# Performance work log

Hardware: AMD Instinct MI355X
Metric: run time of the kernel (lower is better)

The kernel has to match this reference:

```python
import jax, jax.numpy as jnp
import numpy as np

THRESHOLD = 0.9
N = 20000
K = 32
F = 64


def setup_inputs() -> dict:
    key = jax.random.key(0)
    k1, k2, k3, k4, k5 = jax.random.split(key, 5)
    features = jax.random.normal(k1, (N, F), dtype=jnp.float32)
    score = jax.random.normal(k2, (N, 1), dtype=jnp.float32)
    distances = jax.random.uniform(k3, (N, K), dtype=jnp.float32)
    # two equal segments; neighbours sampled within own segment, self at col 0
    row_splits = jnp.array([0, N // 2, N], dtype=jnp.int32)
    segN = N // 2
    local_self = (jnp.arange(N, dtype=jnp.int32) % segN)
    seg_start = (jnp.arange(N, dtype=jnp.int32) // segN) * segN
    r = jax.random.randint(k4, (N, K - 1), 0, segN - 1, dtype=jnp.int32)
    r = r + (r >= local_self[:, None]).astype(jnp.int32)  # avoid sampling self
    neigh = seg_start[:, None] + r
    nidxs = jnp.concatenate([jnp.arange(N, dtype=jnp.int32)[:, None], neigh], axis=1)
    tidxs = jax.random.randint(k5, (N, 1), 0, 50, dtype=jnp.int32)
    return {"features": features, "score": score, "distances": distances,
            "nidxs": nidxs, "row_splits": row_splits, "tidxs": tidxs}


def _lnc(features, score_logits, nidxs, row_splits):
    n, k = nidxs.shape
    score = jax.nn.sigmoid(score_logits[:, 0])  # [N]
    # hierarchy order: per row-split segment, descending score
    seg_id = jnp.searchsorted(row_splits, jnp.arange(n), side='right') - 1
    order = jnp.lexsort((-score, seg_id))

    arangeK = jnp.arange(k)

    def step(carry, p):
        ggather, sel, npg, gcount = carry
        already = ggather[p] >= 0
        high = score[p] > THRESHOLD
        m = nidxs[p]                                   # [K], m[0] == p (self)
        free = (m >= 0) & (ggather[jnp.clip(m, 0, n - 1)] < 0)
        self_only = arangeK == 0
        valid = jnp.where(high, free, self_only) & (~already) & (m >= 0)
        g = gcount
        idx_w = jnp.where(valid, m, n)                 # dummy slot n for masked writes
        ggather = ggather.at[idx_w].set(g)
        row_i = jnp.where(already, n, g)
        sel = sel.at[row_i].set(jnp.where(valid, m, -1))
        npg = npg.at[row_i].set(jnp.sum(valid.astype(jnp.int32)))
        created = (~already).astype(jnp.int32)
        return (ggather, sel, npg, gcount + created), created

    init = (jnp.full((n + 1,), -1, jnp.int32),
            jnp.full((n + 1, k), -1, jnp.int32),
            jnp.zeros((n + 1,), jnp.int32),
            jnp.int32(0))
    (ggather, sel, npg, gcount), created = jax.lax.scan(step, init, order)
    ggather, sel, npg = ggather[:n], sel[:n], npg[:n]

    # new row splits: cumulative group count at segment boundaries
    cum = jnp.cumsum(created)
    rs_new = jnp.concatenate([jnp.zeros((1,), jnp.int32),
                              cum[row_splits[1:] - 1].astype(jnp.int32)])

    # pooled features per group (rows >= gcount are padding)
    sel_c = jnp.clip(sel, 0, n - 1)
    gathered = features[sel_c]                         # [N, K, F]
    mask = (sel >= 0)[..., None]
    out_mean = jnp.sum(jnp.where(mask, gathered, 0.0), axis=1)
    out_mean = out_mean / (npg[:, None].astype(features.dtype) + 1e-6)
    out_max = jnp.max(jnp.where(mask, gathered, -1000.0), axis=1)
    out = jnp.concatenate([out_mean, out_max], axis=-1)  # [N, 2F]
    backgather = ggather[:, None]
    return out, rs_new, backgather


def reference(features, score, distances, nidxs, row_splits, tidxs):
    # distances/tidxs only feed the (disabled) loss branch; kept for signature parity
    return _lnc(features, score, nidxs, row_splits)
```

## Files before the change

kernel.cpp:

```cpp
#include <hip/hip_runtime.h>


constexpr int KN = 32;
constexpr int FD = 64;
constexpr int HOCAP = 512;
constexpr int EW = 16;
constexpr int NBB = 2048;
constexpr int NT = 256;
constexpr int NMAX = 20000;
constexpr int BSLOT = 64;

typedef unsigned long long u64;


__global__ void k0_init(const float* __restrict__ score, float* __restrict__ s,
                        int* __restrict__ grab, u64* __restrict__ hlkStage,
                        int* __restrict__ hcnt, int* __restrict__ lcnt0,
                        int* __restrict__ lcnt1, u64* __restrict__ key,
                        const int* __restrict__ row_splits, int n) {
  __shared__ int ch, cl0, cl1;
  int tid = (int)threadIdx.x, bid = (int)blockIdx.x;
  int x = bid * NT + tid;
  int lane = tid & 63;
  int half = row_splits[1];
  if (tid == 0) { ch = 0; cl0 = 0; cl1 = 0; }
  __syncthreads();
  bool hi = false, lo = false;
  u64 pk = 0;
  if (x < n) {
    float sp = 1.0f / (1.0f + expf(-score[x]));
    s[x] = sp; grab[x] = 0x7FFFFFFF;
    hi = sp > 0.9f; lo = !hi;
    unsigned sb = __float_as_uint(sp);
    pk = ((u64)(x >= half) << 63) | ((u64)(0x7FFFFFFFu - sb) << 32) | (unsigned)x;
    key[x] = lo ? (((u64)sb << 32) | (u64)(0xFFFFFFFFu - (unsigned)x)) : 0ull;
  }
  u64 bh = __ballot(hi);
  u64 b0 = __ballot(lo && x < half);
  u64 b1 = __ballot(lo && x >= half);
  int base = 0;
  if (lane == 0) {
    if (bh) base = atomicAdd(&ch, __popcll(bh));
    if (b0) atomicAdd(&cl0, __popcll(b0));
    if (b1) atomicAdd(&cl1, __popcll(b1));
  }
  base = __shfl(base, 0);
  if (hi) {
    int idx = base + __popcll(bh & ((1ull << lane) - 1ull));
    if (idx < BSLOT) hlkStage[bid * BSLOT + idx] = pk;
  }
  __syncthreads();
  if (tid == 0) {
    hcnt[bid] = (ch > BSLOT) ? BSLOT : ch;
    lcnt0[bid] = cl0; lcnt1[bid] = cl1;
  }
}

__global__ __launch_bounds__(1024, 1) void kA(
    const u64* __restrict__ hlkStage, const int* __restrict__ hcnt,
    const int* __restrict__ lcnt0, const int* __restrict__ lcnt1,
    const int* __restrict__ nidxs, const int* __restrict__ row_splits,
    int* __restrict__ nbm, int* __restrict__ fgj, int* __restrict__ counters,
    int n) {
  __shared__ unsigned short hr16[NMAX];
  __shared__ unsigned E[HOCAP * EW];
  __shared__ u64 hk[HOCAP];
  __shared__ int hol[HOCAP];
  __shared__ int fgjL[HOCAP];
  __shared__ int cnts[128];
  __shared__ int pref[129];
  __shared__ int lsum[2];
  __shared__ int shg;
  int tid = (int)threadIdx.x;
  int lane = tid & 63;
  int half = row_splits[1];
  int nblk = (n + NT - 1) / NT; if (nblk > 128) nblk = 128;

  {
    unsigned* h32 = (unsigned*)hr16;
    for (int i = tid; i < NMAX / 2; i += 1024) h32[i] = 0xFFFFFFFFu;
  }
  for (int i = tid; i < HOCAP * EW; i += 1024) E[i] = 0u;
  if (tid < 128) cnts[tid] = (tid < nblk) ? hcnt[tid] : 0;
  if (tid == 0) { lsum[0] = 0; lsum[1] = 0; }
  __syncthreads();

  if (tid < 64) {
    int v0 = cnts[tid], v1 = cnts[64 + tid];
#pragma unroll
    for (int off = 1; off < 64; off <<= 1) {
      int t0 = __shfl_up(v0, off), t1 = __shfl_up(v1, off);
      if (lane >= off) { v0 += t0; v1 += t1; }
    }
    int s0 = __shfl(v0, 63);
    pref[tid + 1] = v0;
    pref[64 + tid + 1] = v1 + s0;
    if (tid == 0) pref[0] = 0;
  }
  if (tid >= 64 && tid < 192) {
    int b = tid - 64;
    if (b < nblk) { atomicAdd(&lsum[0], lcnt0[b]); atomicAdd(&lsum[1], lcnt1[b]); }
  }
  __syncthreads();
  int nh = pref[nblk]; if (nh > HOCAP) nh = HOCAP;

  for (int t = tid; t < nblk * BSLOT; t += 1024) {
    int b = t >> 6, j = t & (BSLOT - 1);
    if (j < cnts[b]) {
      int d = pref[b] + j;
      if (d < HOCAP) hk[d] = hlkStage[t];
    }
  }
  __syncthreads();

  for (int i = tid; i < nh; i += 1024) {
    u64 kp = hk[i];
    int rk = 0;
#pragma unroll 8
    for (int j = 0; j < nh; ++j) rk += (hk[j] < kp) ? 1 : 0;
    int p = (int)(unsigned)(kp & 0xFFFFFFFFu);
    hol[rk] = p; hr16[p] = (unsigned short)rk;
  }
  __syncthreads();

  {
    const int4* nsrc = (const int4*)nidxs;
    int4* ndstG = (int4*)nbm;
    int tot = nh * 8;
    for (int t = tid; t < tot; t += 1024) {
      int j = t >> 3, q4 = t & 7;
      int p = hol[j];
      int4 v = nsrc[p * 8 + q4];
      ndstG[t] = v;
      unsigned bit = 1u << (j & 31);
      unsigned widx = (unsigned)(j >> 5);
      int xs[4] = { v.x, v.y, v.z, v.w };
#pragma unroll
      for (int e = 0; e < 4; ++e) {
        unsigned r = ((unsigned)xs[e] < (unsigned)n) ? hr16[xs[e]] : 0xFFFFu;
        if (r != 0xFFFFu) atomicOr(&E[r * EW + widx], bit);
      }
    }
  }
  __syncthreads();

  if (tid < 64) {
    unsigned Fw[16];
#pragma unroll
    for (int w = 0; w < 16; ++w) Fw[w] = 0u;
    int hg = 0, h0 = 0, h1 = 0;
    u64 mask_lt = (1ull << lane) - 1ull;
#pragma unroll
    for (int c = 0; c < HOCAP / 64; ++c) {
      if (c * 64 >= nh) break;
      int j = c * 64 + lane;
      bool valid = j < nh;
      unsigned er[16];
#pragma unroll
      for (int w = 0; w < 16; ++w) er[w] = valid ? E[j * EW + w] : 0u;
      unsigned acc = 0;
#pragma unroll
      for (int w = 0; w < 16; ++w) acc |= er[w] & Fw[w];
      bool base_already = acc != 0u;
      u64 erc = ((u64)er[2 * c + 1] << 32) | er[2 * c];
      u64 fb = 0;
      for (int l = 0; l < 64; ++l) {
        bool already = base_already || ((erc & fb) != 0ull);
        bool formed = valid && !already;
        fb |= __ballot(formed && (lane == l));
      }
      Fw[2 * c]     |= (unsigned)(fb & 0xFFFFFFFFull);
      Fw[2 * c + 1] |= (unsigned)(fb >> 32);
      bool formed = (fb >> lane) & 1ull;
      int p = valid ? hol[j] : 0;
      if (formed) {
        int idx = hg + __popcll(fb & mask_lt);
        fgjL[idx] = j;
      }
      h0 += __popcll(__ballot(formed && p < half));
      h1 += __popcll(__ballot(formed && p >= half));
      hg += __popcll(fb);
    }
    if (lane == 0) {
      counters[1] = hg; counters[2] = h0; counters[3] = h1; shg = hg;
    }
  }
  __syncthreads();
  int hg = shg;
  for (int i = tid; i < hg; i += 1024) fgj[i] = fgjL[i];
  if (tid == 0) {
    counters[0] = nh;
    counters[4] = lsum[0];
    counters[5] = lsum[1];
  }
}

__global__ void kG(const float* __restrict__ s, const int* __restrict__ nbm,
                   const int* __restrict__ fgj, int* __restrict__ grab,
                   u64* __restrict__ key, int* __restrict__ counters,
                   const int* __restrict__ row_splits, int n) {
  int t = (int)(blockIdx.x * blockDim.x + threadIdx.x);
  int lane = (int)threadIdx.x & 63;
  int half = row_splits[1];
  int hg = counters[1];
  bool gl0 = false, gl1 = false;
  if (t < hg * KN) {
    int g = t >> 5;
    int x = nbm[fgj[g] * KN + (t & 31)];
    if ((unsigned)x < (unsigned)n) {
      int old = atomicMin(&grab[x], g);
      if (old == 0x7FFFFFFF && !(s[x] > 0.9f)) {
        key[x] = 0ull;
        if (x < half) gl0 = true; else gl1 = true;
      }
    }
  }
  u64 b0 = __ballot(gl0), b1 = __ballot(gl1);
  if (lane == 0) {
    if (b0) atomicSub(&counters[4], __popcll(b0));
    if (b1) atomicSub(&counters[5], __popcll(b1));
  }
}

__global__ void kBC(const int* __restrict__ row_splits, const u64* __restrict__ key,
                    const int* __restrict__ grab, const int* __restrict__ nbm,
                    const int* __restrict__ fgj, const int* __restrict__ counters,
                    const float* __restrict__ feat, float* __restrict__ out,
                    int n, int rs_off) {
  int tid = (int)threadIdx.x, bid = (int)blockIdx.x;
  int gtid = bid * NT + tid;
  int lane = tid & 63;
  int half = row_splits[1];
  const int GSZ = NBB * NT;
  const int NW = GSZ >> 6;
  int wid = gtid >> 6;
  int hg = counters[1], H0 = counters[2], H1 = counters[3];
  int L0 = counters[4], L1 = counters[5];
  int G = H0 + H1 + L0 + L1;
  int bg = rs_off + 3;
  const float inv1 = 1.0f / (1.0f + 1e-6f);

  for (int x = gtid; x < n; x += GSZ) {
    int prov = grab[x];
    if (prov != 0x7FFFFFFF)
      out[bg + x] = (float)((prov < H0) ? prov : (prov + L0));
  }

  for (int row = G + wid; row < n; row += NW) {
    out[row * (2 * FD) + lane] = 0.0f;
    out[row * (2 * FD) + FD + lane] = -1000.0f;
  }

  for (int tsk = wid; tsk < ((n + 3) >> 2); tsk += NW) {
    int p0 = tsk * 4;
    u64 kp0 = key[p0];
    u64 kp1 = (p0 + 1 < n) ? key[p0 + 1] : 0ull;
    u64 kp2 = (p0 + 2 < n) ? key[p0 + 2] : 0ull;
    u64 kp3 = (p0 + 3 < n) ? key[p0 + 3] : 0ull;
    if ((kp0 | kp1 | kp2 | kp3) == 0ull) continue;
    int base2 = (p0 < half) ? 0 : (half >> 1);
    int npair = ((p0 < half) ? half : (n - half)) >> 1;
    const ulonglong2* key2 = (const ulonglong2*)key;
    unsigned r0 = 0, r1 = 0, r2 = 0, r3 = 0;
    for (int j = lane; j < npair; j += 64) {
      ulonglong2 kk = key2[base2 + j];
      r0 += (unsigned)((kk.x > kp0) + (kk.y > kp0));
      r1 += (unsigned)((kk.x > kp1) + (kk.y > kp1));
      r2 += (unsigned)((kk.x > kp2) + (kk.y > kp2));
      r3 += (unsigned)((kk.x > kp3) + (kk.y > kp3));
    }
#pragma unroll
    for (int off = 32; off > 0; off >>= 1) {
      r0 += __shfl_down(r0, off);
      r1 += __shfl_down(r1, off);
      r2 += __shfl_down(r2, off);
      r3 += __shfl_down(r3, off);
    }
    r0 = __shfl(r0, 0); r1 = __shfl(r1, 0); r2 = __shfl(r2, 0); r3 = __shfl(r3, 0);
    unsigned rr[4] = { r0, r1, r2, r3 };
    u64 kps[4] = { kp0, kp1, kp2, kp3 };
#pragma unroll
    for (int j = 0; j < 4; ++j) {
      if (kps[j] == 0ull) continue;
      int p = p0 + j;
      int base = (p < half) ? H0 : (H0 + L0 + H1);
      int gid = base + (int)rr[j];
      float v = feat[p * FD + lane];
      out[gid * (2 * FD) + lane] = v * inv1;
      out[gid * (2 * FD) + FD + lane] = v;
      if (lane == 0) out[bg + p] = (float)gid;
    }
  }

  for (int g = wid; g < hg; g += NW) {
    int x = 0;
    bool mine = false;
    if (lane < KN) {
      x = nbm[fgj[g] * KN + lane];
      mine = (grab[x] == g);
    }
    u64 bal = __ballot(mine);
    unsigned mask = (unsigned)(bal & 0xFFFFFFFFull);
    int npg = __popc(mask);
    float sum = 0.0f, mx = -1000.0f;
    for (int k = 0; k < KN; ++k) {
      if (mask & (1u << k)) {
        int m = __shfl(x, k);
        float v = feat[m * FD + lane];
        sum += v; mx = fmaxf(mx, v);
      }
    }
    int gid2 = (g < H0) ? g : (g + L0);
    out[gid2 * (2 * FD) + lane] = sum / ((float)npg + 1e-6f);
    out[gid2 * (2 * FD) + FD + lane] = mx;
  }

  if (gtid == 0) {
    out[rs_off + 0] = 0.0f;
    out[rs_off + 1] = (float)(H0 + L0);
    out[rs_off + 2] = (float)(H0 + L0 + H1 + L1);
  }
}

extern "C" void kernel_launch(void* const* d_in, const int* in_sizes, int n_in,
                              void* d_out, int out_size, void* d_ws, size_t ws_size,
                              hipStream_t stream) {
  const float* features   = (const float*)d_in[0];
  const float* score      = (const float*)d_in[1];
  const int*   nidxs      = (const int*)d_in[3];
  const int*   row_splits = (const int*)d_in[4];
  int n = in_sizes[1];
  float* out = (float*)d_out;
  int* wsi = (int*)d_ws;
  int rs_off = n * 2 * FD;

  int*      counters = wsi;
  float*    s        = (float*)(wsi + 8);
  int*      grab     = wsi + 8 + n;
  u64*      key      = (u64*)(wsi + 8 + 2 * n);
  int*      nbm      = wsi + 8 + 5 * n;
  int*      fgj      = wsi + 8 + 5 * n + HOCAP * KN;
  u64*      hlkStage = (u64*)(fgj + 2 * HOCAP);
  int*      hcnt     = (int*)(hlkStage + 128 * BSLOT);
  int*      lcnt0    = hcnt + 128;
  int*      lcnt1    = lcnt0 + 128;

  int blocks = (n + NT - 1) / NT;
  k0_init<<<blocks, NT, 0, stream>>>(score, s, grab, hlkStage, hcnt, lcnt0,
                                     lcnt1, key, row_splits, n);
  kA<<<1, 1024, 0, stream>>>(hlkStage, hcnt, lcnt0, lcnt1, nidxs, row_splits,
                             nbm, fgj, counters, n);
  kG<<<(HOCAP * KN) / NT, NT, 0, stream>>>(s, nbm, fgj, grab, key, counters,
                                           row_splits, n);
  kBC<<<NBB, NT, 0, stream>>>(row_splits, key, grab, nbm, fgj, counters,
                              features, out, n, rs_off);
}
```

Before: 74.32 us.

## Stage segment keys in LDS tiles for rank counting and reorder group pooling

The rank-counting phase now works per block: 16 points (4 per wave) share a key tile loaded cooperatively into swizzled shared memory, instead of each wave streaming the whole segment from global memory. The high-score group pooling loop moves ahead of the ranking loop and is assigned to waves from the last block backward, to balance load across blocks. In exchange, every block now sweeps the full segment even when all its keys are zero, and the ranking loop adds __syncthreads barriers.

```diff
diff --git a/kernel.cpp b/kernel.cpp
--- a/kernel.cpp
+++ b/kernel.cpp
@@ -9,9 +9,11 @@
 constexpr int NT = 256;
 constexpr int NMAX = 20000;
 constexpr int BSLOT = 64;
+constexpr int TS = 2048;
 
 typedef unsigned long long u64;
 
+__device__ __forceinline__ int swz(int i) { return i ^ ((i >> 4) & 3); }
 
 __global__ void k0_init(const float* __restrict__ score, float* __restrict__ s,
                         int* __restrict__ grab, u64* __restrict__ hlkStage,
@@ -227,9 +229,11 @@
                     const int* __restrict__ fgj, const int* __restrict__ counters,
                     const float* __restrict__ feat, float* __restrict__ out,
                     int n, int rs_off) {
+  __shared__ u64 ktile[TS];
   int tid = (int)threadIdx.x, bid = (int)blockIdx.x;
   int gtid = bid * NT + tid;
   int lane = tid & 63;
+  int wv = tid >> 6;
   int half = row_splits[1];
   const int GSZ = NBB * NT;
   const int NW = GSZ >> 6;
@@ -251,23 +255,54 @@
     out[row * (2 * FD) + FD + lane] = -1000.0f;
   }
 
-  for (int tsk = wid; tsk < ((n + 3) >> 2); tsk += NW) {
-    int p0 = tsk * 4;
-    u64 kp0 = key[p0];
-    u64 kp1 = (p0 + 1 < n) ? key[p0 + 1] : 0ull;
-    u64 kp2 = (p0 + 2 < n) ? key[p0 + 2] : 0ull;
-    u64 kp3 = (p0 + 3 < n) ? key[p0 + 3] : 0ull;
-    if ((kp0 | kp1 | kp2 | kp3) == 0ull) continue;
-    int base2 = (p0 < half) ? 0 : (half >> 1);
-    int npair = ((p0 < half) ? half : (n - half)) >> 1;
-    const ulonglong2* key2 = (const ulonglong2*)key;
+  {
+    int wtail = (NBB - 1 - bid) * (NT >> 6) + wv;
+    for (int g = wtail; g < hg; g += NW) {
+      int x = 0;
+      bool mine = false;
+      if (lane < KN) {
+        x = nbm[fgj[g] * KN + lane];
+        mine = (grab[x] == g);
+      }
+      u64 bal = __ballot(mine);
+      unsigned mask = (unsigned)(bal & 0xFFFFFFFFull);
+      int npg = __popc(mask);
+      float sum = 0.0f, mx = -1000.0f;
+      for (int k = 0; k < KN; ++k) {
+        if (mask & (1u << k)) {
+          int m = __shfl(x, k);
+          float v = feat[m * FD + lane];
+          sum += v; mx = fmaxf(mx, v);
+        }
+      }
+      int gid2 = (g < H0) ? g : (g + L0);
+      out[gid2 * (2 * FD) + lane] = sum / ((float)npg + 1e-6f);
+      out[gid2 * (2 * FD) + FD + lane] = mx;
+    }
+  }
+
+  int nblk16 = (n + 15) >> 4;
+  for (int tsk = bid; tsk < nblk16; tsk += NBB) {
+    int p0 = tsk * 16;
+    int pw = p0 + wv * 4;
+    u64 kp[4];
+#pragma unroll
+    for (int j = 0; j < 4; ++j) kp[j] = (pw + j < n) ? key[pw + j] : 0ull;
+    int seg_lo = (p0 < half) ? 0 : half;
+    int seg_cnt = (p0 < half) ? half : (n - half);
     unsigned r0 = 0, r1 = 0, r2 = 0, r3 = 0;
-    for (int j = lane; j < npair; j += 64) {
-      ulonglong2 kk = key2[base2 + j];
-      r0 += (unsigned)((kk.x > kp0) + (kk.y > kp0));
-      r1 += (unsigned)((kk.x > kp1) + (kk.y > kp1));
-      r2 += (unsigned)((kk.x > kp2) + (kk.y > kp2));
-      r3 += (unsigned)((kk.x > kp3) + (kk.y > kp3));
+    for (int toff = 0; toff < seg_cnt; toff += TS) {
+      int tcnt = seg_cnt - toff; if (tcnt > TS) tcnt = TS;
+      __syncthreads();
+      for (int i = tid; i < tcnt; i += NT) ktile[swz(i)] = key[seg_lo + toff + i];
+      __syncthreads();
+      for (int i = lane; i < tcnt; i += 64) {
+        u64 kk = ktile[swz(i)];
+        r0 += (kk > kp[0]) ? 1u : 0u;
+        r1 += (kk > kp[1]) ? 1u : 0u;
+        r2 += (kk > kp[2]) ? 1u : 0u;
+        r3 += (kk > kp[3]) ? 1u : 0u;
+      }
     }
 #pragma unroll
     for (int off = 32; off > 0; off >>= 1) {
@@ -278,11 +313,10 @@
     }
     r0 = __shfl(r0, 0); r1 = __shfl(r1, 0); r2 = __shfl(r2, 0); r3 = __shfl(r3, 0);
     unsigned rr[4] = { r0, r1, r2, r3 };
-    u64 kps[4] = { kp0, kp1, kp2, kp3 };
 #pragma unroll
     for (int j = 0; j < 4; ++j) {
-      if (kps[j] == 0ull) continue;
-      int p = p0 + j;
+      if (kp[j] == 0ull) continue;
+      int p = pw + j;
       int base = (p < half) ? H0 : (H0 + L0 + H1);
       int gid = base + (int)rr[j];
       float v = feat[p * FD + lane];
@@ -290,29 +324,6 @@
       out[gid * (2 * FD) + FD + lane] = v;
       if (lane == 0) out[bg + p] = (float)gid;
     }
-  }
-
-  for (int g = wid; g < hg; g += NW) {
-    int x = 0;
-    bool mine = false;
-    if (lane < KN) {
-      x = nbm[fgj[g] * KN + lane];
-      mine = (grab[x] == g);
-    }
-    u64 bal = __ballot(mine);
-    unsigned mask = (unsigned)(bal & 0xFFFFFFFFull);
-    int npg = __popc(mask);
-    float sum = 0.0f, mx = -1000.0f;
-    for (int k = 0; k < KN; ++k) {
-      if (mask & (1u << k)) {
-        int m = __shfl(x, k);
-        float v = feat[m * FD + lane];
-        sum += v; mx = fmaxf(mx, v);
-      }
-    }
-    int gid2 = (g < H0) ? g : (g + L0);
-    out[gid2 * (2 * FD) + lane] = sum / ((float)npg + 1e-6f);
-    out[gid2 * (2 * FD) + FD + lane] = mx;
   }
 
   if (gtid == 0) {
```

After: 69.99 us (median of 3 runs). 5.8% less time.
